# Optimization experiments

Hardware: AMD Instinct MI355X
Metric: run time of the kernel (lower is better)

Reference implementation:

```python
import jax, jax.numpy as jnp
import numpy as np

B, GS, IN_H, GCN_H, LIN_H = 65536, 7, 5, 144, 128


def _xavier(key, shape):
    fan_in, fan_out = shape[0], shape[1]
    limit = np.sqrt(6.0 / (fan_in + fan_out)).astype(np.float32)
    return jax.random.uniform(key, shape, jnp.float32, -limit, limit)


def setup_inputs() -> dict:
    key = jax.random.key(0)
    ks = jax.random.split(key, 12)
    operations = jax.random.normal(ks[0], (B, GS, IN_H), jnp.float32)
    adjacency = (jax.random.uniform(ks[1], (B, GS, GS)) < 0.3).astype(jnp.float32)
    num_vertices = jax.random.randint(ks[2], (B,), 1, 8).astype(jnp.float32)
    w1_0 = _xavier(ks[3], (IN_H, GCN_H))
    w2_0 = _xavier(ks[4], (IN_H, GCN_H))
    w1_1 = _xavier(ks[5], (GCN_H, GCN_H))
    w2_1 = _xavier(ks[6], (GCN_H, GCN_H))
    w1_2 = _xavier(ks[7], (GCN_H, GCN_H))
    w2_2 = _xavier(ks[8], (GCN_H, GCN_H))
    fc1_w = _xavier(ks[9], (LIN_H, GCN_H))  # torch Linear stores [out, in]
    fc2_w = _xavier(ks[10], (1, LIN_H))
    return {
        'operations': operations, 'adjacency': adjacency, 'num_vertices': num_vertices,
        'w1_0': w1_0, 'w2_0': w2_0, 'w1_1': w1_1, 'w2_1': w2_1,
        'w1_2': w1_2, 'w2_2': w2_2, 'fc1_w': fc1_w, 'fc2_w': fc2_w,
    }


def _row_normalize(adj):
    # divide each row by its sum (matches torch normalize_adj)
    return adj / adj.sum(axis=2, keepdims=True)


def reference(operations, adjacency, num_vertices,
              w1_0, w2_0, w1_1, w2_1, w1_2, w2_2, fc1_w, fc2_w):
    gs = adjacency.shape[1]
    eye = jnp.eye(gs, dtype=adjacency.dtype)
    adj_d = _row_normalize(adjacency + eye)  # [B, gs, gs]
    x = operations
    for w1, w2 in ((w1_0, w2_0), (w1_1, w2_1), (w1_2, w2_2)):
        norm_adj = _row_normalize(adj_d)                      # identity in value, kept faithful
        inv_norm_adj = _row_normalize(adj_d.transpose(0, 2, 1))
        o1 = jax.nn.relu(jnp.einsum('bij,bjk->bik', norm_adj, x @ w1))
        o2 = jax.nn.relu(jnp.einsum('bij,bjk->bik', inv_norm_adj, x @ w2))
        x = (o1 + o2) * 0.5  # dropout is identity at inference
    pooled = x.sum(axis=1) / num_vertices[:, None]            # [B, gcn_hidden]
    h = pooled @ fc1_w.T                                      # [B, linear_hidden]
    out = (h @ fc2_w.T).reshape(-1)                           # [B]
    return out
```

## Files before the change

### kernel.cpp

```cpp
#include <hip/hip_runtime.h>


typedef _Float16 half8   __attribute__((ext_vector_type(8)));
typedef _Float16 half4_t __attribute__((ext_vector_type(4)));
typedef _Float16 half2_t __attribute__((ext_vector_type(2)));
typedef float    floatx16 __attribute__((ext_vector_type(16)));

constexpr int GS = 7;
constexpr int NI = 8;
constexpr int MROWS = NI * GS;
constexpr int H = 144;
constexpr int LSTRIDE = 81 * 512;
constexpr int WT_HALFS = 3 * LSTRIDE;

static __device__ inline half8 bc(_Float16 v) {
    half8 h = {v, v, v, v, v, v, v, v};
    return h;
}

__global__ void prep_kernel(const float* __restrict__ w10, const float* __restrict__ w20,
                            const float* __restrict__ w11, const float* __restrict__ w21,
                            const float* __restrict__ w12, const float* __restrict__ w22,
                            const float* __restrict__ fc1, const float* __restrict__ fc2,
                            _Float16* __restrict__ wt, float* __restrict__ g)
{
    const int gidx = blockIdx.x * 256 + threadIdx.x;
    if (gidx < WT_HALFS) {
        const int l    = gidx / LSTRIDE;
        const int r    = gidx - l * LSTRIDE;
        const int frag = r >> 9;
        const int wi   = r & 511;
        const int lane = wi >> 3;
        const int j8   = wi & 7;
        const int c    = frag / 27;
        const int rem  = frag - c * 27;
        const int t    = rem / 9;
        const int ks   = rem - t * 9;
        const int n    = c * 96 + t * 32 + (lane & 31);
        const int k    = ks * 16 + (lane >> 5) * 8 + j8;
        const int jw   = n >> 1;
        const int p    = n & 1;
        const float* W = (l == 0) ? (p ? w20 : w10)
                       : (l == 1) ? (p ? w21 : w11)
                                  : (p ? w22 : w12);
        const int K = (l == 0) ? 5 : 144;
        wt[gidx] = (k < K) ? (_Float16)W[k * H + jw] : (_Float16)0.f;
    }
    if (blockIdx.x == WT_HALFS / 256 && threadIdx.x < H) {
        const int j = threadIdx.x;
        float s = 0.f;
        for (int o = 0; o < 128; ++o) s = fmaf(fc2[o], fc1[o * H + j], s);
        g[j] = s;
    }
}

__global__ __launch_bounds__(256, 5)
void gcn_mfma(const float* __restrict__ ops, const float* __restrict__ adj,
              const float* __restrict__ nv,
              const _Float16* __restrict__ wt, const float* __restrict__ gw,
              float* __restrict__ out)
{
    __shared__ __align__(16) _Float16 sX[64][152];
    __shared__ __align__(16) _Float16 sT[MROWS][104];

    _Float16 (*sA)[2][GS][8] = (_Float16(*)[2][GS][8])&sX[MROWS][0];
    float (*adjd)[GS][GS] = (float(*)[GS][GS])&sT[0][0];

    const int tid  = threadIdx.x;
    const int lane = tid & 63;
    const int wv   = tid >> 6;
    const int ibase = blockIdx.x * NI;

    if (tid < MROWS) {
        const int item = tid / GS, r = tid % GS;
        const float* orow = ops + ((size_t)(ibase + item) * GS + r) * 5;
        half8 h = bc((_Float16)0);
        h[0] = (_Float16)orow[0]; h[1] = (_Float16)orow[1]; h[2] = (_Float16)orow[2];
        h[3] = (_Float16)orow[3]; h[4] = (_Float16)orow[4];
        *(half8*)&sX[tid][0] = h;
        *(half8*)&sX[tid][8] = bc((_Float16)0);

        const float* arow = adj + ((size_t)(ibase + item) * GS + r) * GS;
        float a[GS]; float s = 0.f;
        #pragma unroll
        for (int c = 0; c < GS; ++c) { a[c] = arow[c] + (c == r ? 1.f : 0.f); s += a[c]; }
        const float is = 1.f / s;
        #pragma unroll
        for (int c = 0; c < GS; ++c) {
            const float v = a[c] * is;
            adjd[item][r][c] = v;
            sA[item][0][r][c] = (_Float16)v;
        }
        sA[item][0][r][7] = (_Float16)0.f;
    }
    __syncthreads();
    if (tid < MROWS) {
        const int item = tid / GS, r = tid % GS;
        float v[GS]; float s = 0.f;
        #pragma unroll
        for (int k = 0; k < GS; ++k) { v[k] = adjd[item][k][r]; s += v[k]; }
        const float is = 1.f / s;
        #pragma unroll
        for (int k = 0; k < GS; ++k) sA[item][1][r][k] = (_Float16)(v[k] * is);
        sA[item][1][r][7] = (_Float16)0.f;
    }
    __syncthreads();

    const int mt     = wv & 1;
    const int arow31 = lane & 31;
    const int mrow   = mt * 32 + arow31;
    const int khi    = (lane >> 5) * 8;
    const int t0     = (wv < 2) ? 0 : 2;
    const int tcnt   = (wv < 2) ? 2 : 1;

    const int mitem = tid / 24;
    const int mb    = tid - mitem * 24;
    half2_t xr0[GS], xr1[GS];

    for (int layer = 0; layer < 3; ++layer) {
        const int nk = (layer == 0) ? 1 : 9;
        const _Float16* wl = wt + layer * LSTRIDE;

        half8 bf[9];
        #pragma unroll
        for (int ks = 0; ks < 9; ++ks)
            if (ks < nk) bf[ks] = *(const half8*)&sX[mrow][ks * 16 + khi];

        for (int chunk = 0; chunk < 3; ++chunk) {
            const _Float16* fb  = wl + (size_t)(chunk * 27) * 512 + (size_t)lane * 8;
            const _Float16* a0p = fb + (size_t)(t0 * 9) * 512;
            const _Float16* a1p = fb + (size_t)((t0 + 1) * 9) * 512;
            floatx16 acc0, acc1;
            #pragma unroll
            for (int i = 0; i < 16; ++i) { acc0[i] = 0.f; acc1[i] = 0.f; }
            #pragma unroll
            for (int ks = 0; ks < 9; ++ks) {
                if (ks < nk) {
                    const half8 a0 = *(const half8*)(a0p + (size_t)ks * 512);
                    acc0 = __builtin_amdgcn_mfma_f32_32x32x16_f16(a0, bf[ks], acc0, 0, 0, 0);
                    if (tcnt == 2) {
                        const half8 a1 = *(const half8*)(a1p + (size_t)ks * 512);
                        acc1 = __builtin_amdgcn_mfma_f32_32x32x16_f16(a1, bf[ks], acc1, 0, 0, 0);
                    }
                }
            }

            if (chunk) __syncthreads();

            if (mrow < MROWS) {
                #pragma unroll
                for (int ti = 0; ti < 2; ++ti) {
                    if (ti < tcnt) {
                        const floatx16& A = ti ? acc1 : acc0;
                        const int ntl = (t0 + ti) * 32 + 4 * (lane >> 5);
                        #pragma unroll
                        for (int q = 0; q < 4; ++q) {
                            half4_t h;
                            h[0] = (_Float16)A[4 * q + 0];
                            h[1] = (_Float16)A[4 * q + 1];
                            h[2] = (_Float16)A[4 * q + 2];
                            h[3] = (_Float16)A[4 * q + 3];
                            *(half4_t*)&sT[mrow][ntl + 8 * q] = h;
                        }
                    }
                }
            }
            __syncthreads();

            if (tid < 192) {
                const int row0 = mitem * GS;
                half2_t e[GS], o[GS];
                #pragma unroll
                for (int k = 0; k < GS; ++k) {
                    const half4_t c = *(const half4_t*)&sT[row0 + k][mb * 4];
                    e[k] = __builtin_shufflevector(c, c, 0, 2);
                    o[k] = __builtin_shufflevector(c, c, 1, 3);
                }
                #pragma unroll
                for (int i = 0; i < GS; ++i) {
                    const half8 aN = *(const half8*)&sA[mitem][0][i][0];
                    const half8 aI = *(const half8*)&sA[mitem][1][i][0];
                    half2_t s1 = {(_Float16)0, (_Float16)0};
                    half2_t s2 = {(_Float16)0, (_Float16)0};
                    #pragma unroll
                    for (int k = 0; k < GS; ++k) {
                        const half2_t bN = {aN[k], aN[k]};
                        const half2_t bI = {aI[k], aI[k]};
                        s1 += bN * e[k];
                        s2 += bI * o[k];
                    }
                    if (s1[0] < (_Float16)0) s1[0] = (_Float16)0;
                    if (s1[1] < (_Float16)0) s1[1] = (_Float16)0;
                    if (s2[0] < (_Float16)0) s2[0] = (_Float16)0;
                    if (s2[1] < (_Float16)0) s2[1] = (_Float16)0;
                    const half2_t x = (s1 + s2) * (half2_t){(_Float16)0.5f, (_Float16)0.5f};
                    if (chunk == 0)      xr0[i] = x;
                    else if (chunk == 1) xr1[i] = x;
                    else {
                        *(half2_t*)&sX[row0 + i][96 + 2 * mb] = x;
                        *(half2_t*)&sX[row0 + i][      2 * mb] = xr0[i];
                        *(half2_t*)&sX[row0 + i][ 48 + 2 * mb] = xr1[i];
                    }
                }
            }
        }
        __syncthreads();
    }

    if (tid < NI * 16) {
        const int item = tid >> 4, part = tid & 15;
        float s = 0.f;
        #pragma unroll
        for (int c = 0; c < 9; ++c) {
            const int j = part * 9 + c;
            const float gj = gw[j];
            #pragma unroll
            for (int i = 0; i < GS; ++i)
                s = fmaf((float)sX[item * GS + i][j], gj, s);
        }
        s += __shfl_xor(s, 1);
        s += __shfl_xor(s, 2);
        s += __shfl_xor(s, 4);
        s += __shfl_xor(s, 8);
        if (part == 0) out[ibase + item] = s / nv[ibase + item];
    }
}

extern "C" void kernel_launch(void* const* d_in, const int* in_sizes, int n_in,
                              void* d_out, int out_size, void* d_ws, size_t ws_size,
                              hipStream_t stream) {
    const float* ops = (const float*)d_in[0];
    const float* adj = (const float*)d_in[1];
    const float* nv  = (const float*)d_in[2];
    const float* w10 = (const float*)d_in[3];
    const float* w20 = (const float*)d_in[4];
    const float* w11 = (const float*)d_in[5];
    const float* w21 = (const float*)d_in[6];
    const float* w12 = (const float*)d_in[7];
    const float* w22 = (const float*)d_in[8];
    const float* fc1 = (const float*)d_in[9];
    const float* fc2 = (const float*)d_in[10];

    _Float16* wt = (_Float16*)d_ws;
    float*    g  = (float*)((char*)d_ws + (size_t)WT_HALFS * 2);

    prep_kernel<<<WT_HALFS / 256 + 1, 256, 0, stream>>>(w10, w20, w11, w21, w12, w22,
                                                        fc1, fc2, wt, g);
    gcn_mfma<<<65536 / NI, 256, 0, stream>>>(ops, adj, nv, wt, g, (float*)d_out);
}
```

Baseline: 324.4 us.

## Aggregate adjacency before weight GEMM and fuse ReLU-average into MFMA epilogue

Reorders each GCN layer from (A·(X·W)) to ((A·X)·W). The adjacency-normalised and inverse-normalised aggregations are computed first into two new shared buffers, then MFMAs multiply them by W1 and W2 separately. ReLU and the 0.5 average are applied directly on the accumulators, which removes the chunked sT staging pass and its extra barriers. The weight layout is rebuilt into separate non-interleaved W1/W2 fragments padded to 160 columns, which adds some MFMA work. Shared memory grows to three 56x152 buffers, so launch bounds drop from 5 to 3 blocks per CU, trading occupancy for fewer synchronisation phases.

```diff
diff --git a/kernel.cpp b/kernel.cpp
--- a/kernel.cpp
+++ b/kernel.cpp
@@ -3,14 +3,13 @@
 
 typedef _Float16 half8   __attribute__((ext_vector_type(8)));
 typedef _Float16 half4_t __attribute__((ext_vector_type(4)));
-typedef _Float16 half2_t __attribute__((ext_vector_type(2)));
 typedef float    floatx16 __attribute__((ext_vector_type(16)));
 
 constexpr int GS = 7;
 constexpr int NI = 8;
 constexpr int MROWS = NI * GS;
 constexpr int H = 144;
-constexpr int LSTRIDE = 81 * 512;
+constexpr int LSTRIDE = 2 * 5 * 9 * 512;
 constexpr int WT_HALFS = 3 * LSTRIDE;
 
 static __device__ inline half8 bc(_Float16 v) {
@@ -32,19 +31,17 @@
         const int wi   = r & 511;
         const int lane = wi >> 3;
         const int j8   = wi & 7;
-        const int c    = frag / 27;
-        const int rem  = frag - c * 27;
-        const int t    = rem / 9;
-        const int ks   = rem - t * 9;
-        const int n    = c * 96 + t * 32 + (lane & 31);
+        const int p    = frag / 45;
+        const int rem  = frag - p * 45;
+        const int nt   = rem / 9;
+        const int ks   = rem - nt * 9;
+        const int n    = nt * 32 + (lane & 31);
         const int k    = ks * 16 + (lane >> 5) * 8 + j8;
-        const int jw   = n >> 1;
-        const int p    = n & 1;
         const float* W = (l == 0) ? (p ? w20 : w10)
                        : (l == 1) ? (p ? w21 : w11)
                                   : (p ? w22 : w12);
         const int K = (l == 0) ? 5 : 144;
-        wt[gidx] = (k < K) ? (_Float16)W[k * H + jw] : (_Float16)0.f;
+        wt[gidx] = (n < H && k < K) ? (_Float16)W[k * H + n] : (_Float16)0.f;
     }
     if (blockIdx.x == WT_HALFS / 256 && threadIdx.x < H) {
         const int j = threadIdx.x;
@@ -54,17 +51,18 @@
     }
 }
 
-__global__ __launch_bounds__(256, 5)
+__global__ __launch_bounds__(256, 3)
 void gcn_mfma(const float* __restrict__ ops, const float* __restrict__ adj,
               const float* __restrict__ nv,
               const _Float16* __restrict__ wt, const float* __restrict__ gw,
               float* __restrict__ out)
 {
-    __shared__ __align__(16) _Float16 sX[64][152];
-    __shared__ __align__(16) _Float16 sT[MROWS][104];
-
-    _Float16 (*sA)[2][GS][8] = (_Float16(*)[2][GS][8])&sX[MROWS][0];
-    float (*adjd)[GS][GS] = (float(*)[GS][GS])&sT[0][0];
+    __shared__ __align__(16) _Float16 sX [MROWS][152];
+    __shared__ __align__(16) _Float16 sXn[MROWS][152];
+    __shared__ __align__(16) _Float16 sXi[MROWS][152];
+    __shared__ __align__(16) _Float16 sAh[NI][2][GS][8];
+
+    float (*adjd)[GS][GS] = (float(*)[GS][GS])&sXn[0][0];
 
     const int tid  = threadIdx.x;
     const int lane = tid & 63;
@@ -89,9 +87,9 @@
         for (int c = 0; c < GS; ++c) {
             const float v = a[c] * is;
             adjd[item][r][c] = v;
-            sA[item][0][r][c] = (_Float16)v;
-        }
-        sA[item][0][r][7] = (_Float16)0.f;
+            sAh[item][0][r][c] = (_Float16)v;
+        }
+        sAh[item][0][r][7] = (_Float16)0.f;
     }
     __syncthreads();
     if (tid < MROWS) {
@@ -101,105 +99,98 @@
         for (int k = 0; k < GS; ++k) { v[k] = adjd[item][k][r]; s += v[k]; }
         const float is = 1.f / s;
         #pragma unroll
-        for (int k = 0; k < GS; ++k) sA[item][1][r][k] = (_Float16)(v[k] * is);
-        sA[item][1][r][7] = (_Float16)0.f;
+        for (int k = 0; k < GS; ++k) sAh[item][1][r][k] = (_Float16)(v[k] * is);
+        sAh[item][1][r][7] = (_Float16)0.f;
     }
     __syncthreads();
 
     const int mt     = wv & 1;
     const int arow31 = lane & 31;
     const int mrow   = mt * 32 + arow31;
+    const int mrowc  = (mrow < MROWS) ? mrow : 0;
     const int khi    = (lane >> 5) * 8;
-    const int t0     = (wv < 2) ? 0 : 2;
-    const int tcnt   = (wv < 2) ? 2 : 1;
-
-    const int mitem = tid / 24;
-    const int mb    = tid - mitem * 24;
-    half2_t xr0[GS], xr1[GS];
+    const int ntbase = (wv < 2) ? 0 : 3;
+    const int ntcnt  = (wv < 2) ? 3 : 2;
 
     for (int layer = 0; layer < 3; ++layer) {
         const int nk = (layer == 0) ? 1 : 9;
-        const _Float16* wl = wt + layer * LSTRIDE;
-
-        half8 bf[9];
-        #pragma unroll
-        for (int ks = 0; ks < 9; ++ks)
-            if (ks < nk) bf[ks] = *(const half8*)&sX[mrow][ks * 16 + khi];
-
-        for (int chunk = 0; chunk < 3; ++chunk) {
-            const _Float16* fb  = wl + (size_t)(chunk * 27) * 512 + (size_t)lane * 8;
-            const _Float16* a0p = fb + (size_t)(t0 * 9) * 512;
-            const _Float16* a1p = fb + (size_t)((t0 + 1) * 9) * 512;
-            floatx16 acc0, acc1;
+        const _Float16* wl = wt + (size_t)layer * LSTRIDE;
+
+        if (layer == 0) {
+            for (int u = tid; u < MROWS * 2; u += 256) {
+                const int row = u >> 1, cb = u & 1;
+                const int item = row / GS, rr = row - item * GS;
+                const int c0 = cb * 8;
+                const half8 aN = *(const half8*)&sAh[item][0][rr][0];
+                const half8 aI = *(const half8*)&sAh[item][1][rr][0];
+                half8 an = bc((_Float16)0), ai = bc((_Float16)0);
+                #pragma unroll
+                for (int j = 0; j < GS; ++j) {
+                    const half8 xj = *(const half8*)&sX[item * GS + j][c0];
+                    an += bc(aN[j]) * xj;
+                    ai += bc(aI[j]) * xj;
+                }
+                *(half8*)&sXn[row][c0] = an;
+                *(half8*)&sXi[row][c0] = ai;
+            }
+        } else {
+            for (int u = tid; u < MROWS * 18; u += 256) {
+                const int row = u / 18, cb = u - row * 18;
+                const int item = row / GS, rr = row - item * GS;
+                const int c0 = cb * 8;
+                const half8 aN = *(const half8*)&sAh[item][0][rr][0];
+                const half8 aI = *(const half8*)&sAh[item][1][rr][0];
+                half8 an = bc((_Float16)0), ai = bc((_Float16)0);
+                #pragma unroll
+                for (int j = 0; j < GS; ++j) {
+                    const half8 xj = *(const half8*)&sX[item * GS + j][c0];
+                    an += bc(aN[j]) * xj;
+                    ai += bc(aI[j]) * xj;
+                }
+                *(half8*)&sXn[row][c0] = an;
+                *(half8*)&sXi[row][c0] = ai;
+            }
+        }
+        __syncthreads();
+
+        half8 bn[9], bi[9];
+        #pragma unroll
+        for (int ks = 0; ks < 9; ++ks) {
+            if (ks < nk) {
+                bn[ks] = *(const half8*)&sXn[mrowc][ks * 16 + khi];
+                bi[ks] = *(const half8*)&sXi[mrowc][ks * 16 + khi];
+            }
+        }
+
+        for (int t = 0; t < ntcnt; ++t) {
+            const int nt = ntbase + t;
+            const _Float16* a1p = wl + (size_t)(nt * 9) * 512 + (size_t)lane * 8;
+            const _Float16* a2p = a1p + (size_t)(45 * 512);
+            floatx16 acc1, acc2;
             #pragma unroll
-            for (int i = 0; i < 16; ++i) { acc0[i] = 0.f; acc1[i] = 0.f; }
+            for (int i = 0; i < 16; ++i) { acc1[i] = 0.f; acc2[i] = 0.f; }
             #pragma unroll
             for (int ks = 0; ks < 9; ++ks) {
                 if (ks < nk) {
-                    const half8 a0 = *(const half8*)(a0p + (size_t)ks * 512);
-                    acc0 = __builtin_amdgcn_mfma_f32_32x32x16_f16(a0, bf[ks], acc0, 0, 0, 0);
-                    if (tcnt == 2) {
-                        const half8 a1 = *(const half8*)(a1p + (size_t)ks * 512);
-                        acc1 = __builtin_amdgcn_mfma_f32_32x32x16_f16(a1, bf[ks], acc1, 0, 0, 0);
-                    }
-                }
-            }
-
-            if (chunk) __syncthreads();
-
+                    const half8 a1 = *(const half8*)(a1p + (size_t)ks * 512);
+                    acc1 = __builtin_amdgcn_mfma_f32_32x32x16_f16(a1, bn[ks], acc1, 0, 0, 0);
+                    const half8 a2 = *(const half8*)(a2p + (size_t)ks * 512);
+                    acc2 = __builtin_amdgcn_mfma_f32_32x32x16_f16(a2, bi[ks], acc2, 0, 0, 0);
+                }
+            }
             if (mrow < MROWS) {
                 #pragma unroll
-                for (int ti = 0; ti < 2; ++ti) {
-                    if (ti < tcnt) {
-                        const floatx16& A = ti ? acc1 : acc0;
-                        const int ntl = (t0 + ti) * 32 + 4 * (lane >> 5);
+                for (int q = 0; q < 4; ++q) {
+                    const int n0 = nt * 32 + 4 * (lane >> 5) + 8 * q;
+                    if (n0 < H) {
+                        half4_t h;
                         #pragma unroll
-                        for (int q = 0; q < 4; ++q) {
-                            half4_t h;
-                            h[0] = (_Float16)A[4 * q + 0];
-                            h[1] = (_Float16)A[4 * q + 1];
-                            h[2] = (_Float16)A[4 * q + 2];
-                            h[3] = (_Float16)A[4 * q + 3];
-                            *(half4_t*)&sT[mrow][ntl + 8 * q] = h;
+                        for (int i = 0; i < 4; ++i) {
+                            const float v1 = acc1[4 * q + i] > 0.f ? acc1[4 * q + i] : 0.f;
+                            const float v2 = acc2[4 * q + i] > 0.f ? acc2[4 * q + i] : 0.f;
+                            h[i] = (_Float16)(0.5f * (v1 + v2));
                         }
-                    }
-                }
-            }
-            __syncthreads();
-
-            if (tid < 192) {
-                const int row0 = mitem * GS;
-                half2_t e[GS], o[GS];
-                #pragma unroll
-                for (int k = 0; k < GS; ++k) {
-                    const half4_t c = *(const half4_t*)&sT[row0 + k][mb * 4];
-                    e[k] = __builtin_shufflevector(c, c, 0, 2);
-                    o[k] = __builtin_shufflevector(c, c, 1, 3);
-                }
-                #pragma unroll
-                for (int i = 0; i < GS; ++i) {
-                    const half8 aN = *(const half8*)&sA[mitem][0][i][0];
-                    const half8 aI = *(const half8*)&sA[mitem][1][i][0];
-                    half2_t s1 = {(_Float16)0, (_Float16)0};
-                    half2_t s2 = {(_Float16)0, (_Float16)0};
-                    #pragma unroll
-                    for (int k = 0; k < GS; ++k) {
-                        const half2_t bN = {aN[k], aN[k]};
-                        const half2_t bI = {aI[k], aI[k]};
-                        s1 += bN * e[k];
-                        s2 += bI * o[k];
-                    }
-                    if (s1[0] < (_Float16)0) s1[0] = (_Float16)0;
-                    if (s1[1] < (_Float16)0) s1[1] = (_Float16)0;
-                    if (s2[0] < (_Float16)0) s2[0] = (_Float16)0;
-                    if (s2[1] < (_Float16)0) s2[1] = (_Float16)0;
-                    const half2_t x = (s1 + s2) * (half2_t){(_Float16)0.5f, (_Float16)0.5f};
-                    if (chunk == 0)      xr0[i] = x;
-                    else if (chunk == 1) xr1[i] = x;
-                    else {
-                        *(half2_t*)&sX[row0 + i][96 + 2 * mb] = x;
-                        *(half2_t*)&sX[row0 + i][      2 * mb] = xr0[i];
-                        *(half2_t*)&sX[row0 + i][ 48 + 2 * mb] = xr1[i];
+                        *(half4_t*)&sX[mrow][n0] = h;
                     }
                 }
             }
```

Result: faster. 280.6 us (-13.5%).
